# Kernel tuning notes

Hardware: AMD Instinct MI355X
Metric: run time of the kernel (lower is better)

Reference implementation:

```python
import jax, jax.numpy as jnp
import numpy as np

B, N, O, K, F = 4, 256, 5, 5, 256
H, D, DFF = 4, 64, 1024  # num_heads, KQ_len, FFN hidden
EPS = 1e-5


def setup_inputs() -> dict:
    key = jax.random.key(0)
    ks = jax.random.split(key, 16)
    s = 0.05
    p = lambda k, shape: (jax.random.normal(k, shape, jnp.float32) * s)
    return {
        "x": jax.random.normal(ks[0], (B, N, O, K, K, F), jnp.float32),
        "Wq": p(ks[1], (H * D, F)), "bq": p(ks[2], (H * D,)),
        "Wk": p(ks[3], (H * D, F)), "bk": p(ks[4], (H * D,)),
        "Wv": p(ks[5], (H * D, F)), "bv": p(ks[6], (H * D,)),
        "Wf": p(ks[7], (F, F)), "bf": p(ks[8], (F,)),
        "ln1_w": jnp.ones((N, O, F), jnp.float32), "ln1_b": jnp.zeros((N, O, F), jnp.float32),
        "ln2_w": jnp.ones((N, O, F), jnp.float32), "ln2_b": jnp.zeros((N, O, F), jnp.float32),
        "W1": p(ks[9], (DFF, F)), "b1": p(ks[10], (DFF,)),
        "W2": p(ks[11], (F, DFF)), "b2": p(ks[12], (F,)),
    }


def _layer_norm3(x, w, b):
    # torch LayerNorm with normalized_shape=[N, O, F]: stats over last 3 dims
    mu = jnp.mean(x, axis=(1, 2, 3), keepdims=True)
    var = jnp.var(x, axis=(1, 2, 3), keepdims=True)
    return (x - mu) * jax.lax.rsqrt(var + EPS) * w + b


def _split_heads(y):
    # [B,N,O,K,K,H*D] -> [B,N,O,H,K,K,D]
    return y.reshape(B, N, O, K, K, H, D).transpose(0, 1, 2, 5, 3, 4, 6)


def reference(x, Wq, bq, Wk, bk, Wv, bv, Wf, bf,
              ln1_w, ln1_b, ln2_w, ln2_b, W1, b1, W2, b2):
    q = _split_heads(x @ Wq.T + bq)
    k = _split_heads(x @ Wk.T + bk)
    v = _split_heads(x @ Wv.T + bv)
    c = K // 2
    qc = q[:, :, :, :, c, c, :]  # center query [B,N,O,H,D]
    # tile+mul+sum == dot of center query against every patch key
    scores = jnp.einsum('bnohd,bnohijd->bnohij', qc, k) / np.sqrt(float(D))
    w = jax.nn.softmax(scores.reshape(B, N, O, H, K * K), axis=-1)
    merged = jnp.einsum('bnohp,bnohpd->bnohd', w, v.reshape(B, N, O, H, K * K, D))
    merged = merged.reshape(B, N, O, H * D)
    attent = merged @ Wf.T + bf  # dropout = identity (eval)
    out1 = _layer_norm3(attent, ln1_w, ln1_b)
    ffn = jax.nn.relu(out1 @ W1.T + b1) @ W2.T + b2
    return _layer_norm3(out1 + ffn, ln2_w, ln2_b)
```

## Files before the change

### kernel.cpp

```cpp
#include <hip/hip_runtime.h>
#include <hip/hip_bf16.h>

#define FF 256
#define HH 4
#define DD 64
#define PP 25
#define SITES 5120
#define SPB 1280
#define DFF 1024
#define LN_ELEMS 327680

typedef const __hip_bfloat16* bfp;
typedef __hip_bfloat16* bfw;
typedef __attribute__((ext_vector_type(8))) short bf16x8;
typedef __attribute__((ext_vector_type(4))) float f32x4;

__device__ __forceinline__ float b2f(const __hip_bfloat16 v) { return __bfloat162float(v); }
__device__ __forceinline__ bool detect_bf(const unsigned* dt) {
    return dt[0] == 0x3F803F80u;
}
__device__ __forceinline__ float ldin(const void* p, size_t i, bool bf) {
    return bf ? __bfloat162float(((const __hip_bfloat16*)p)[i]) : ((const float*)p)[i];
}
__device__ __forceinline__ unsigned short f2bu(float f) {
    __hip_bfloat16 h = __float2bfloat16(f);
    return *(unsigned short*)&h;
}
__device__ __forceinline__ uint4 ldin8(const void* p, size_t i, bool bf) {
    if (bf) return *(const uint4*)((const unsigned short*)p + i);
    const float* f = (const float*)p + i;
    const float4 a = *(const float4*)f;
    const float4 b = *(const float4*)(f + 4);
    unsigned short u[8] = { f2bu(a.x), f2bu(a.y), f2bu(a.z), f2bu(a.w),
                            f2bu(b.x), f2bu(b.y), f2bu(b.z), f2bu(b.w) };
    return *(uint4*)u;
}

template<int RELU, int RES, int GATHER, int STATS, int BINT, int OUTF32>
__global__ __launch_bounds__(256) void gemm_mfma(
    const void* xg, bfp Ab, int lda,
    const void* Bm, int ldb, const void* bias,
    bfp resid, int ldr, bfw C, int ldc, int Kc,
    int aoh, size_t boh, int bioh, int coh,
    float* __restrict__ red, const unsigned* dt)
{
    const bool bf = detect_bf(dt);
    const int h = blockIdx.z;
    Ab += (size_t)h * aoh;
    const size_t boff = (size_t)h * boh;
    const size_t biasoff = (size_t)h * bioh;
    C += (size_t)h * coh;

    __shared__ unsigned short Als[64][72];
    __shared__ unsigned short Bls[64][72];
    __shared__ float rs4[4], rss4[4];
    const int tid = threadIdx.x;
    const int lane = tid & 63;
    const int w = tid >> 6;
    const int m0 = blockIdx.y * 64;
    const int n0 = blockIdx.x * 64;
    const int r8 = tid >> 3;
    const int c8 = (tid & 7) * 8;

    f32x4 acc[4];
    #pragma unroll
    for (int mi = 0; mi < 4; ++mi) acc[mi] = (f32x4){0.f, 0.f, 0.f, 0.f};

    for (int k0 = 0; k0 < Kc; k0 += 64) {
        #pragma unroll
        for (int rr = 0; rr < 2; ++rr) {
            const int row = r8 + rr * 32;
            uint4 v;
            if (GATHER) v = ldin8(xg, ((size_t)(m0 + row) * PP + 12) * FF + (k0 + c8), bf);
            else        v = *(const uint4*)(Ab + (size_t)(m0 + row) * lda + (k0 + c8));
            *(uint4*)&Als[row][c8] = v;
        }
        #pragma unroll
        for (int rr = 0; rr < 2; ++rr) {
            const int row = r8 + rr * 32;
            const size_t bi = boff + (size_t)(n0 + row) * ldb + (k0 + c8);
            uint4 v;
            if (BINT) v = *(const uint4*)((const unsigned short*)Bm + bi);
            else      v = ldin8(Bm, bi, bf);
            *(uint4*)&Bls[row][c8] = v;
        }
        __syncthreads();
        #pragma unroll
        for (int ks = 0; ks < 2; ++ks) {
            const int kq = ks * 32 + (lane >> 4) * 8;
            const bf16x8 bfr = *(const bf16x8*)&Bls[w * 16 + (lane & 15)][kq];
            #pragma unroll
            for (int mi = 0; mi < 4; ++mi) {
                const bf16x8 afr = *(const bf16x8*)&Als[mi * 16 + (lane & 15)][kq];
                acc[mi] = __builtin_amdgcn_mfma_f32_16x16x32_bf16(afr, bfr, acc[mi], 0, 0, 0);
            }
        }
        __syncthreads();
    }

    const int col = n0 + w * 16 + (lane & 15);
    const int quad = lane >> 4;
    const float bvv = (!OUTF32 && bias) ? ldin(bias, biasoff + col, bf) : 0.f;
    float s_ = 0.f, ss_ = 0.f;
    #pragma unroll
    for (int mi = 0; mi < 4; ++mi) {
        #pragma unroll
        for (int r = 0; r < 4; ++r) {
            const int row = m0 + mi * 16 + quad * 4 + r;
            float v = acc[mi][r] + bvv;
            if (OUTF32) {
                ((float*)C)[(size_t)row * ldc + col] = v;
            } else {
                if (RES)  v += b2f(resid[(size_t)row * ldr + col]);
                if (RELU) v = fmaxf(v, 0.0f);
                if (STATS) { s_ += v; ss_ += v * v; }
                C[(size_t)row * ldc + col] = __float2bfloat16(v);
            }
        }
    }
    if (STATS && !OUTF32) {
        #pragma unroll
        for (int o = 32; o > 0; o >>= 1) { s_ += __shfl_down(s_, o); ss_ += __shfl_down(ss_, o); }
        if (lane == 0) { rs4[w] = s_; rss4[w] = ss_; }
        __syncthreads();
        if (tid == 0) {
            const int batch = m0 / SPB;
            atomicAdd(&red[batch * 2 + 0], rs4[0] + rs4[1] + rs4[2] + rs4[3]);
            atomicAdd(&red[batch * 2 + 1], rss4[0] + rss4[1] + rss4[2] + rss4[3]);
        }
    }
}

__global__ __launch_bounds__(256) void prep(
    const void* Wq, const void* Wk, const void* Wv, const void* Wf,
    const void* W1, const void* W2,
    bfw WkT, bfw Wqb, bfw Wvb, bfw Wfb, bfw W1b, bfw W2b,
    float* __restrict__ red, const unsigned* dt)
{
    const bool bf = detect_bf(dt);
    if (blockIdx.x == 0 && threadIdx.x < 16) red[threadIdx.x] = 0.f;
    const int idx = blockIdx.x * 256 + threadIdx.x;
    if (idx < 65536) {
        const int d = idx & 63, f = (idx >> 6) & 255, h = idx >> 14;
        WkT[idx] = __float2bfloat16(ldin(Wk, (size_t)(h * DD + d) * FF + f, bf));
    } else if (idx < 131072) {
        const int i = idx - 65536;  Wqb[i] = __float2bfloat16(ldin(Wq, i, bf));
    } else if (idx < 196608) {
        const int i = idx - 131072; Wvb[i] = __float2bfloat16(ldin(Wv, i, bf));
    } else if (idx < 262144) {
        const int i = idx - 196608; Wfb[i] = __float2bfloat16(ldin(Wf, i, bf));
    } else if (idx < 524288) {
        const int i = idx - 262144; W1b[i] = __float2bfloat16(ldin(W1, i, bf));
    } else {
        const int i = idx - 524288; W2b[i] = __float2bfloat16(ldin(W2, i, bf));
    }
}

__global__ __launch_bounds__(256) void ffn2_epi(
    const float* __restrict__ zp, bfp out1, const void* b2, bfw z,
    float* __restrict__ red, const unsigned* dt)
{
    const bool bf = detect_bf(dt);
    __shared__ float rs4[4], rss4[4];
    const int tid = threadIdx.x;
    const int i8 = (blockIdx.x * 256 + tid) * 8;
    const int col = i8 & 255;
    float v[8];
    #pragma unroll
    for (int j = 0; j < 8; ++j) v[j] = 0.f;
    #pragma unroll
    for (int kc = 0; kc < 4; ++kc) {
        const float4 a = *(const float4*)(zp + (size_t)kc * (SITES * FF) + i8);
        const float4 b = *(const float4*)(zp + (size_t)kc * (SITES * FF) + i8 + 4);
        v[0] += a.x; v[1] += a.y; v[2] += a.z; v[3] += a.w;
        v[4] += b.x; v[5] += b.y; v[6] += b.z; v[7] += b.w;
    }
    const uint4 rv = *(const uint4*)(out1 + i8);
    const unsigned short* ru = (const unsigned short*)&rv;
    float s_ = 0.f, ss_ = 0.f;
    unsigned short ou[8];
    #pragma unroll
    for (int j = 0; j < 8; ++j) {
        const float val = v[j] + ldin(b2, col + j, bf)
                        + __bfloat162float(*(const __hip_bfloat16*)&ru[j]);
        s_ += val; ss_ += val * val;
        ou[j] = f2bu(val);
    }
    *(uint4*)((unsigned short*)z + i8) = *(uint4*)ou;
    const int lane = tid & 63, w = tid >> 6;
    #pragma unroll
    for (int o = 32; o > 0; o >>= 1) { s_ += __shfl_down(s_, o); ss_ += __shfl_down(ss_, o); }
    if (lane == 0) { rs4[w] = s_; rss4[w] = ss_; }
    __syncthreads();
    if (tid == 0) {
        const int batch = (i8 >> 8) / SPB;
        atomicAdd(&red[batch * 2 + 0], rs4[0] + rs4[1] + rs4[2] + rs4[3]);
        atomicAdd(&red[batch * 2 + 1], rss4[0] + rss4[1] + rss4[2] + rss4[3]);
    }
}

__global__ __launch_bounds__(256) void attn_site(const void* x, bfp qk, bfw xw,
                                                 const unsigned* dt)
{
    __shared__ unsigned short xsb[32][264];
    __shared__ unsigned short qkb[HH][FF];
    __shared__ float sc[HH][32];
    __shared__ float wl[HH][PP];

    const bool bf = detect_bf(dt);
    const int s = blockIdx.x;
    const int t = threadIdx.x;

    const size_t xbase = (size_t)s * (PP * FF);
    for (int e0 = t * 8; e0 < PP * FF; e0 += 2048)
        *(uint4*)&xsb[e0 >> 8][e0 & 255] = ldin8(x, xbase + e0, bf);
    if (t < 128)
        ((uint4*)qkb)[t] = ((const uint4*)(qk + (size_t)s * (HH * FF)))[t];
    __syncthreads();

    if (t < 64) {
        const int lane = t;
        const int col = lane & 15;
        const int quad = lane >> 4;
        const int brow = col & 3;
        f32x4 a0v = (f32x4){0.f, 0.f, 0.f, 0.f};
        f32x4 a1v = (f32x4){0.f, 0.f, 0.f, 0.f};
        #pragma unroll
        for (int ks = 0; ks < 8; ++ks) {
            const int kq = ks * 32 + quad * 8;
            const bf16x8 bfr = *(const bf16x8*)&qkb[brow][kq];
            const bf16x8 af0 = *(const bf16x8*)&xsb[col][kq];
            const bf16x8 af1 = *(const bf16x8*)&xsb[16 + col][kq];
            a0v = __builtin_amdgcn_mfma_f32_16x16x32_bf16(af0, bfr, a0v, 0, 0, 0);
            a1v = __builtin_amdgcn_mfma_f32_16x16x32_bf16(af1, bfr, a1v, 0, 0, 0);
        }
        if (col < HH) {
            #pragma unroll
            for (int r = 0; r < 4; ++r) {
                const int p = quad * 4 + r;
                sc[col][p] = a0v[r] * 0.125f;
                const int p2 = 16 + p;
                if (p2 < PP) sc[col][p2] = a1v[r] * 0.125f;
            }
        }
    }
    __syncthreads();

    if (t < 128) {
        const int hh = t >> 5, p = t & 31;
        const float sv = (p < PP) ? sc[hh][p] : -1e30f;
        float m = sv;
        #pragma unroll
        for (int o = 16; o > 0; o >>= 1) m = fmaxf(m, __shfl_xor(m, o, 32));
        const float e = (p < PP) ? __expf(sv - m) : 0.f;
        float ssum = e;
        #pragma unroll
        for (int o = 16; o > 0; o >>= 1) ssum += __shfl_xor(ssum, o, 32);
        if (p < PP) wl[hh][p] = e / ssum;
    }
    __syncthreads();

    float a0 = 0.f, a1 = 0.f, a2 = 0.f, a3 = 0.f;
    #pragma unroll
    for (int p = 0; p < PP; ++p) {
        const float xv = __bfloat162float(*(const __hip_bfloat16*)&xsb[p][t]);
        a0 = fmaf(wl[0][p], xv, a0);
        a1 = fmaf(wl[1][p], xv, a1);
        a2 = fmaf(wl[2][p], xv, a2);
        a3 = fmaf(wl[3][p], xv, a3);
    }
    bfw xwp = xw + (size_t)s * (HH * FF) + t;
    xwp[0 * FF] = __float2bfloat16(a0);
    xwp[1 * FF] = __float2bfloat16(a1);
    xwp[2 * FF] = __float2bfloat16(a2);
    xwp[3 * FF] = __float2bfloat16(a3);
}

template<int FINAL>
__global__ __launch_bounds__(256) void ln_apply(bfp X, const float* __restrict__ red,
                                                const void* w, const void* b,
                                                void* out, const unsigned* dt)
{
    const bool bf = detect_bf(dt);
    const int i8 = (blockIdx.x * 256 + threadIdx.x) * 8;
    const int s = i8 >> 8;
    const int batch = s / SPB;
    const int r = s - batch * SPB;
    const int f = i8 & 255;
    const float inv = 1.f / (float)LN_ELEMS;
    const float mu = red[batch * 2] * inv;
    const float var = red[batch * 2 + 1] * inv - mu * mu;
    const float rs = rsqrtf(var + 1e-5f);

    const uint4 xv = *(const uint4*)(X + i8);
    const uint4 wv = ldin8(w, (size_t)r * FF + f, bf);
    const uint4 bv = ldin8(b, (size_t)r * FF + f, bf);
    const unsigned short* xu = (const unsigned short*)&xv;
    const unsigned short* wu = (const unsigned short*)&wv;
    const unsigned short* bu = (const unsigned short*)&bv;
    float vo[8];
    #pragma unroll
    for (int j = 0; j < 8; ++j) {
        const float xf = __bfloat162float(*(const __hip_bfloat16*)&xu[j]);
        const float wf = __bfloat162float(*(const __hip_bfloat16*)&wu[j]);
        const float bf2 = __bfloat162float(*(const __hip_bfloat16*)&bu[j]);
        vo[j] = (xf - mu) * rs * wf + bf2;
    }
    if (FINAL && !bf) {
        float* o = (float*)out + i8;
        *(float4*)o = (float4){vo[0], vo[1], vo[2], vo[3]};
        *(float4*)(o + 4) = (float4){vo[4], vo[5], vo[6], vo[7]};
    } else {
        unsigned short ou[8];
        #pragma unroll
        for (int j = 0; j < 8; ++j) ou[j] = f2bu(vo[j]);
        *(uint4*)((unsigned short*)out + i8) = *(uint4*)ou;
    }
}

extern "C" void kernel_launch(void* const* d_in, const int* in_sizes, int n_in,
                              void* d_out, int out_size, void* d_ws, size_t ws_size,
                              hipStream_t stream)
{
    const void* x    = d_in[0];
    const void* Wq   = d_in[1];
    const void* bq   = d_in[2];
    const void* Wk   = d_in[3];
    const void* Wv   = d_in[5];
    const void* bv   = d_in[6];
    const void* Wf   = d_in[7];
    const void* bfv  = d_in[8];
    const void* ln1w = d_in[9];
    const void* ln1b = d_in[10];
    const void* ln2w = d_in[11];
    const void* ln2b = d_in[12];
    const void* W1   = d_in[13];
    const void* b1   = d_in[14];
    const void* W2   = d_in[15];
    const void* b2   = d_in[16];
    const unsigned* dt = (const unsigned*)d_in[9];

    char* w8 = (char*)d_ws;
    bfw qk   = (bfw)(w8);
    bfw xw   = (bfw)(w8 + 10485760);
    bfw hid  = (bfw)(w8 + 20971520);
    bfw WkT  = (bfw)(w8 + 31457280);
    bfw Wqb  = (bfw)(w8 + 31588352);
    bfw Wvb  = (bfw)(w8 + 31719424);
    bfw Wfb  = (bfw)(w8 + 31850496);
    bfw W1b  = (bfw)(w8 + 31981568);
    bfw W2b  = (bfw)(w8 + 32505856);
    bfw qc   = (bfw)(w8 + 33030144);
    bfw att  = (bfw)(w8 + 35651584);
    bfw out1 = (bfw)(w8 + 38273024);
    bfw z    = (bfw)(w8 + 40894464);
    float* red = (float*)(w8 + 43515904);
    float* zp  = (float*)(w8 + 44040192);

    prep<<<3072, 256, 0, stream>>>(Wq, Wk, Wv, Wf, W1, W2,
                                   WkT, Wqb, Wvb, Wfb, W1b, W2b, red, dt);

    gemm_mfma<0, 0, 1, 0, 1, 0><<<dim3(4, 80), 256, 0, stream>>>(
        x, nullptr, 0, Wqb, FF, bq, nullptr, 0, qc, FF, FF, 0, 0, 0, 0, nullptr, dt);

    gemm_mfma<0, 0, 0, 0, 1, 0><<<dim3(4, 80, HH), 256, 0, stream>>>(
        nullptr, qc, FF, WkT, DD, nullptr, nullptr, 0, qk, HH * FF, DD,
        DD, (size_t)FF * DD, 0, FF, nullptr, dt);

    attn_site<<<SITES, 256, 0, stream>>>(x, qk, xw, dt);

    gemm_mfma<0, 0, 0, 0, 1, 0><<<dim3(1, 80, HH), 256, 0, stream>>>(
        nullptr, xw, HH * FF, Wvb, FF, bv, nullptr, 0, qc, FF, FF,
        FF, (size_t)DD * FF, DD, DD, nullptr, dt);

    gemm_mfma<0, 0, 0, 1, 1, 0><<<dim3(4, 80), 256, 0, stream>>>(
        nullptr, qc, FF, Wfb, FF, bfv, nullptr, 0, att, FF, FF,
        0, 0, 0, 0, red, dt);

    ln_apply<0><<<640, 256, 0, stream>>>(att, red, ln1w, ln1b, out1, dt);

    gemm_mfma<1, 0, 0, 0, 1, 0><<<dim3(16, 80), 256, 0, stream>>>(
        nullptr, out1, FF, W1b, FF, b1, nullptr, 0, hid, DFF, FF,
        0, 0, 0, 0, nullptr, dt);

    gemm_mfma<0, 0, 0, 0, 1, 1><<<dim3(4, 80, 4), 256, 0, stream>>>(
        nullptr, hid, DFF, W2b, DFF, nullptr, nullptr, 0, (bfw)zp, FF, 256,
        256, 256, 0, SITES * FF * 2, nullptr, dt);

    ffn2_epi<<<640, 256, 0, stream>>>(zp, out1, b2, z, red + 8, dt);

    ln_apply<1><<<640, 256, 0, stream>>>(z, red + 8, ln2w, ln2b, d_out, dt);
}
```

Measured before the change: 324.9 us.

## Fuse FFN2 epilogue and final LayerNorm via cooperative grid sync

Merges the FFN2 split-K reduction and residual epilogue with the final LayerNorm into one cooperative kernel. A grid-wide sync waits for the per-batch sum and sum-of-squares atomics, then the values still held in registers are normalized. This drops one kernel launch and the bf16 write and reread of the intermediate z tensor. In exchange it needs a cooperative launch, with all 640 blocks resident at once, and pays for a grid barrier.

```diff
diff --git a/kernel.cpp b/kernel.cpp
--- a/kernel.cpp
+++ b/kernel.cpp
@@ -1,5 +1,6 @@
 #include <hip/hip_runtime.h>
 #include <hip/hip_bf16.h>
+#include <hip/hip_cooperative_groups.h>
 
 #define FF 256
 #define HH 4
@@ -156,9 +157,10 @@
     }
 }
 
-__global__ __launch_bounds__(256) void ffn2_epi(
-    const float* __restrict__ zp, bfp out1, const void* b2, bfw z,
-    float* __restrict__ red, const unsigned* dt)
+__global__ __launch_bounds__(256) void ffn2_ln2(
+    const float* __restrict__ zp, bfp out1, const void* b2,
+    const void* lnw, const void* lnb,
+    float* __restrict__ red, void* out, const unsigned* dt)
 {
     const bool bf = detect_bf(dt);
     __shared__ float rs4[4], rss4[4];
@@ -178,24 +180,56 @@
     const uint4 rv = *(const uint4*)(out1 + i8);
     const unsigned short* ru = (const unsigned short*)&rv;
     float s_ = 0.f, ss_ = 0.f;
-    unsigned short ou[8];
     #pragma unroll
     for (int j = 0; j < 8; ++j) {
-        const float val = v[j] + ldin(b2, col + j, bf)
-                        + __bfloat162float(*(const __hip_bfloat16*)&ru[j]);
-        s_ += val; ss_ += val * val;
-        ou[j] = f2bu(val);
-    }
-    *(uint4*)((unsigned short*)z + i8) = *(uint4*)ou;
+        v[j] += ldin(b2, col + j, bf)
+              + __bfloat162float(*(const __hip_bfloat16*)&ru[j]);
+        s_ += v[j]; ss_ += v[j] * v[j];
+    }
     const int lane = tid & 63, w = tid >> 6;
     #pragma unroll
     for (int o = 32; o > 0; o >>= 1) { s_ += __shfl_down(s_, o); ss_ += __shfl_down(ss_, o); }
     if (lane == 0) { rs4[w] = s_; rss4[w] = ss_; }
     __syncthreads();
+    const int batch = (i8 >> 8) / SPB;
     if (tid == 0) {
-        const int batch = (i8 >> 8) / SPB;
         atomicAdd(&red[batch * 2 + 0], rs4[0] + rs4[1] + rs4[2] + rs4[3]);
         atomicAdd(&red[batch * 2 + 1], rss4[0] + rss4[1] + rss4[2] + rss4[3]);
+    }
+
+    cooperative_groups::this_grid().sync();
+
+    const float sum = __hip_atomic_load(&red[batch * 2 + 0], __ATOMIC_ACQUIRE,
+                                        __HIP_MEMORY_SCOPE_AGENT);
+    const float ssq = __hip_atomic_load(&red[batch * 2 + 1], __ATOMIC_ACQUIRE,
+                                        __HIP_MEMORY_SCOPE_AGENT);
+    const float inv = 1.f / (float)LN_ELEMS;
+    const float mu = sum * inv;
+    const float var = ssq * inv - mu * mu;
+    const float rstd = rsqrtf(var + 1e-5f);
+
+    const int s = i8 >> 8;
+    const int r = s - batch * SPB;
+    const uint4 wv = ldin8(lnw, (size_t)r * FF + col, bf);
+    const uint4 bv = ldin8(lnb, (size_t)r * FF + col, bf);
+    const unsigned short* wu = (const unsigned short*)&wv;
+    const unsigned short* bu = (const unsigned short*)&bv;
+    float vo[8];
+    #pragma unroll
+    for (int j = 0; j < 8; ++j) {
+        const float wf = __bfloat162float(*(const __hip_bfloat16*)&wu[j]);
+        const float bb = __bfloat162float(*(const __hip_bfloat16*)&bu[j]);
+        vo[j] = (v[j] - mu) * rstd * wf + bb;
+    }
+    if (!bf) {
+        float* o = (float*)out + i8;
+        *(float4*)o = (float4){vo[0], vo[1], vo[2], vo[3]};
+        *(float4*)(o + 4) = (float4){vo[4], vo[5], vo[6], vo[7]};
+    } else {
+        unsigned short ou[8];
+        #pragma unroll
+        for (int j = 0; j < 8; ++j) ou[j] = f2bu(vo[j]);
+        *(uint4*)((unsigned short*)out + i8) = *(uint4*)ou;
     }
 }
 
@@ -276,10 +310,9 @@
     xwp[3 * FF] = __float2bfloat16(a3);
 }
 
-template<int FINAL>
 __global__ __launch_bounds__(256) void ln_apply(bfp X, const float* __restrict__ red,
                                                 const void* w, const void* b,
-                                                void* out, const unsigned* dt)
+                                                bfw out, const unsigned* dt)
 {
     const bool bf = detect_bf(dt);
     const int i8 = (blockIdx.x * 256 + threadIdx.x) * 8;
@@ -298,24 +331,15 @@
     const unsigned short* xu = (const unsigned short*)&xv;
     const unsigned short* wu = (const unsigned short*)&wv;
     const unsigned short* bu = (const unsigned short*)&bv;
-    float vo[8];
+    unsigned short ou[8];
     #pragma unroll
     for (int j = 0; j < 8; ++j) {
         const float xf = __bfloat162float(*(const __hip_bfloat16*)&xu[j]);
         const float wf = __bfloat162float(*(const __hip_bfloat16*)&wu[j]);
         const float bf2 = __bfloat162float(*(const __hip_bfloat16*)&bu[j]);
-        vo[j] = (xf - mu) * rs * wf + bf2;
-    }
-    if (FINAL && !bf) {
-        float* o = (float*)out + i8;
-        *(float4*)o = (float4){vo[0], vo[1], vo[2], vo[3]};
-        *(float4*)(o + 4) = (float4){vo[4], vo[5], vo[6], vo[7]};
-    } else {
-        unsigned short ou[8];
-        #pragma unroll
-        for (int j = 0; j < 8; ++j) ou[j] = f2bu(vo[j]);
-        *(uint4*)((unsigned short*)out + i8) = *(uint4*)ou;
-    }
+        ou[j] = f2bu((xf - mu) * rs * wf + bf2);
+    }
+    *(uint4*)((unsigned short*)out + i8) = *(uint4*)ou;
 }
 
 extern "C" void kernel_launch(void* const* d_in, const int* in_sizes, int n_in,
@@ -353,7 +377,6 @@
     bfw qc   = (bfw)(w8 + 33030144);
     bfw att  = (bfw)(w8 + 35651584);
     bfw out1 = (bfw)(w8 + 38273024);
-    bfw z    = (bfw)(w8 + 40894464);
     float* red = (float*)(w8 + 43515904);
     float* zp  = (float*)(w8 + 44040192);
 
@@ -377,7 +400,7 @@
         nullptr, qc, FF, Wfb, FF, bfv, nullptr, 0, att, FF, FF,
         0, 0, 0, 0, red, dt);
 
-    ln_apply<0><<<640, 256, 0, stream>>>(att, red, ln1w, ln1b, out1, dt);
+    ln_apply<<<640, 256, 0, stream>>>(att, red, ln1w, ln1b, out1, dt);
 
     gemm_mfma<1, 0, 0, 0, 1, 0><<<dim3(16, 80), 256, 0, stream>>>(
         nullptr, out1, FF, W1b, FF, b1, nullptr, 0, hid, DFF, FF,
@@ -387,7 +410,19 @@
         nullptr, hid, DFF, W2b, DFF, nullptr, nullptr, 0, (bfw)zp, FF, 256,
         256, 256, 0, SITES * FF * 2, nullptr, dt);
 
-    ffn2_epi<<<640, 256, 0, stream>>>(zp, out1, b2, z, red + 8, dt);
-
-    ln_apply<1><<<640, 256, 0, stream>>>(z, red + 8, ln2w, ln2b, d_out, dt);
-}
+    {
+        const float* zp_c = zp;
+        bfp out1_c = out1;
+        float* red8 = red + 8;
+        void* outp = d_out;
+        const unsigned* dtp = dt;
+        const void* b2p = b2;
+        const void* lnwp = ln2w;
+        const void* lnbp = ln2b;
+        void* args[] = { (void*)&zp_c, (void*)&out1_c, (void*)&b2p,
+                         (void*)&lnwp, (void*)&lnbp,
+                         (void*)&red8, (void*)&outp, (void*)&dtp };
+        hipLaunchCooperativeKernel((void*)ffn2_ln2, dim3(640), dim3(256),
+                                   args, 0, stream);
+    }
+}
```

Result: slower. 433.5 us (+33.4%).
